# Performance work log

Measured on AMD Instinct MI355X. Metric: run time of the kernel, lower is better.

Reference implementation:

```python
import jax, jax.numpy as jnp
import numpy as np

N_HEAD = 16
ROPE_BASE = 10000.0


def _rotate_half(x):
    # interleaved rotate: (-x2, x1) pairs, matching torch stack+flatten
    x1 = x[..., ::2]
    x2 = x[..., 1::2]
    return jnp.stack((-x2, x1), axis=-1).reshape(x.shape)


def setup_inputs() -> dict:
    key = jax.random.key(0)
    ks = jax.random.split(key, 5)
    B, S, C = 4, 2048, 1024
    sc = 1.0 / np.sqrt(C)
    return {
        "x": jax.random.normal(ks[0], (B, S, C), jnp.float32),
        "W_qkv": jax.random.normal(ks[1], (C, 3 * C), jnp.float32) * sc,
        "b_qkv": jax.random.normal(ks[2], (3 * C,), jnp.float32) * 0.02,
        "W_proj": jax.random.normal(ks[3], (C, C), jnp.float32) * sc,
        "b_proj": jax.random.normal(ks[4], (C,), jnp.float32) * 0.02,
    }


def reference(x, W_qkv, b_qkv, W_proj, b_proj):
    B, S, C = x.shape
    H = N_HEAD
    D = C // H

    qkv = x @ W_qkv + b_qkv                       # [B,S,3C]
    q, k, v = jnp.split(qkv, 3, axis=-1)
    q = q.reshape(B, S, H, D).transpose(0, 2, 1, 3)  # [B,H,S,D]
    k = k.reshape(B, S, H, D).transpose(0, 2, 1, 3)
    v = v.reshape(B, S, H, D).transpose(0, 2, 1, 3)

    # RoPE cache (offset=0), faithful to source: emb = cat(freqs, freqs)
    inv_freq = 1.0 / (ROPE_BASE ** (jnp.arange(0, D, 2, dtype=jnp.float32) / D))
    pos = jnp.arange(S, dtype=jnp.float32)
    freqs = jnp.outer(pos, inv_freq)              # [S, D/2]
    emb = jnp.concatenate((freqs, freqs), axis=-1)  # [S, D]
    cos = jnp.cos(emb)[None, None, :, :]
    sin = jnp.sin(emb)[None, None, :, :]

    q = q * cos + _rotate_half(q) * sin
    k = k * cos + _rotate_half(k) * sin

    scale = 1.0 / jnp.sqrt(jnp.asarray(D, x.dtype))
    scores = jnp.einsum("bhqd,bhkd->bhqk", q, k) * scale  # [B,H,S,S]
    causal = jnp.tril(jnp.ones((S, S), dtype=bool))
    scores = jnp.where(causal[None, None], scores, jnp.asarray(-jnp.inf, x.dtype))
    att = jax.nn.softmax(scores, axis=-1)
    out = jnp.einsum("bhqk,bhkd->bhqd", att, v)    # [B,H,S,D]

    out = out.transpose(0, 2, 1, 3).reshape(B, S, C)
    out = out @ W_proj + b_proj                    # dropout=0 (eval)
    return out
```

## Files before the change

kernel.cpp:

```cpp
#include <hip/hip_runtime.h>
#include <hip/hip_bf16.h>
#include <math.h>

#define B_ 4
#define S_ 2048
#define C_ 1024
#define H_ 16
#define D_ 64
#define M_ (B_*S_)
#define NQKV (3*C_)
#define KDIM C_

typedef float f32x4 __attribute__((ext_vector_type(4)));
typedef float f32x16 __attribute__((ext_vector_type(16)));
typedef short bf16x8 __attribute__((ext_vector_type(8)));

static __device__ __forceinline__ ushort f2bf(float f){
    __hip_bfloat16 h = __float2bfloat16(f);
    union { __hip_bfloat16 b; ushort u; } v; v.b = h;
    return v.u;
}

static __device__ __forceinline__ void gload16(const ushort* g, ushort* l){
    __builtin_amdgcn_global_load_lds((__attribute__((address_space(1))) void*)g,
                                     (__attribute__((address_space(3))) void*)l,
                                     16, 0, 0);
}

__global__ void k_prep(const float* __restrict__ x, const float* __restrict__ Wqkv,
                       const float* __restrict__ Wproj,
                       ushort* __restrict__ xb, ushort* __restrict__ wqt,
                       ushort* __restrict__ wpt, unsigned* __restrict__ csT){
    __shared__ float tile[32][33];
    int blk = blockIdx.x, tid = threadIdx.x;
    if (blk < 2048){
        const int n4 = M_*KDIM/4;
        for (int i = blk*256 + tid; i < n4; i += 2048*256){
            float4 v = *(const float4*)(x + (size_t)i*4);
            ushort4 o = { f2bf(v.x), f2bf(v.y), f2bf(v.z), f2bf(v.w) };
            *(ushort4*)(xb + (size_t)i*4) = o;
        }
    } else if (blk < 5120){
        int t = blk - 2048;
        int c0 = (t % 96)*32, r0 = (t / 96)*32;
        int tx = tid & 31, ty = tid >> 5;
        for (int j = ty; j < 32; j += 8)
            tile[j][tx] = Wqkv[(size_t)(r0 + j)*NQKV + c0 + tx];
        __syncthreads();
        for (int j = ty; j < 32; j += 8)
            wqt[(size_t)(c0 + tx)*KDIM + r0 + j] = f2bf(tile[j][tx]);
    } else if (blk < 6144){
        int t = blk - 5120;
        int c0 = (t & 31)*32, r0 = (t >> 5)*32;
        int tx = tid & 31, ty = tid >> 5;
        for (int j = ty; j < 32; j += 8)
            tile[j][tx] = Wproj[(size_t)(r0 + j)*C_ + c0 + tx];
        __syncthreads();
        for (int j = ty; j < 32; j += 8)
            wpt[(size_t)(c0 + tx)*KDIM + r0 + j] = f2bf(tile[j][tx]);
    } else {
        int t = (blk - 6144)*256 + tid;
        int pos = t >> 6, d = t & 63;
        float invf = powf(10000.0f, -(float)(d & 31) / 32.0f);
        float ang = (float)pos * invf;
        csT[t] = (unsigned)f2bf(cosf(ang)) | ((unsigned)f2bf(sinf(ang)) << 16);
    }
}

__launch_bounds__(512, 4)
__global__ void k_qkv(const ushort* __restrict__ xb, const ushort* __restrict__ wt,
                      const float* __restrict__ bqkv, const unsigned* __restrict__ csT,
                      ushort* __restrict__ qb, ushort* __restrict__ kb, ushort* __restrict__ vT){
    __shared__ __align__(16) ushort As[2][256][32];
    __shared__ __align__(16) ushort Bs[2][128][32];
    int bid = blockIdx.x;
    int lin = (bid & 7)*96 + (bid >> 3);
    int bx = lin % 24, by = lin / 24;
    int M0 = by*256, N0 = bx*128;
    int tid = threadIdx.x;
    int wid = tid >> 6, lane = tid & 63;
    int wm = wid >> 1, wn = wid & 1;
    int lrow = lane & 15, lk = lane >> 4;
    int swu = (lrow >> 1) & 3;

    int scol = (((lane & 3) ^ ((lane >> 3) & 3))) * 8;
    const ushort* gA0 = &xb[(size_t)(M0 + wid*16 + (lane >> 2))*KDIM + scol];
    const ushort* gA1 = gA0 + (size_t)128*KDIM;
    const ushort* gB0 = &wt[(size_t)(N0 + wid*16 + (lane >> 2))*KDIM + scol];

    f32x4 acc[4][4] = {};
    int cur = 0;
    gload16(gA0, &As[0][wid*16][0]);
    gload16(gA1, &As[0][128 + wid*16][0]);
    gload16(gB0, &Bs[0][wid*16][0]);
    __syncthreads();

    for (int k0 = 0; k0 < KDIM; k0 += 32){
        int nk = k0 + 32;
        if (nk < KDIM){
            gload16(gA0 + nk, &As[cur^1][wid*16][0]);
            gload16(gA1 + nk, &As[cur^1][128 + wid*16][0]);
            gload16(gB0 + nk, &Bs[cur^1][wid*16][0]);
        }
        bf16x8 a[4], b[4];
#pragma unroll
        for (int mi = 0; mi < 4; mi++)
            a[mi] = *(const bf16x8*)(&As[cur][wm*64 + mi*16 + lrow][(lk ^ swu)*8]);
#pragma unroll
        for (int ni = 0; ni < 4; ni++)
            b[ni] = *(const bf16x8*)(&Bs[cur][wn*64 + ni*16 + lrow][(lk ^ swu)*8]);
#pragma unroll
        for (int mi = 0; mi < 4; mi++)
#pragma unroll
            for (int ni = 0; ni < 4; ni++)
                acc[mi][ni] = __builtin_amdgcn_mfma_f32_16x16x32_bf16(a[mi], b[ni], acc[mi][ni], 0, 0, 0);
        __syncthreads();
        cur ^= 1;
    }
#pragma unroll
    for (int mi = 0; mi < 4; mi++)
#pragma unroll
    for (int ni = 0; ni < 4; ni++){
        int gn = N0 + wn*64 + ni*16 + lrow;
        float bias = bqkv[gn];
        int which = gn >> 10;
        int cn = gn & 1023;
        int h = cn >> 6, d = cn & 63;
        int gm0 = M0 + wm*64 + mi*16 + lk*4;
        int bb = gm0 >> 11, pos0 = gm0 & 2047;
        if (which == 2){
            ushort4 o = { f2bf(acc[mi][ni][0] + bias), f2bf(acc[mi][ni][1] + bias),
                          f2bf(acc[mi][ni][2] + bias), f2bf(acc[mi][ni][3] + bias) };
            *(ushort4*)(&vT[(((size_t)(bb*H_ + h))*D_ + d)*S_ + pos0]) = o;
        } else {
#pragma unroll
            for (int rr = 0; rr < 4; rr++){
                float val = acc[mi][ni][rr] + bias;
                float rot = __shfl_xor(val, 1);
                unsigned cs = csT[(pos0 + rr)*64 + d];
                float c = __uint_as_float(cs << 16);
                float s = __uint_as_float(cs & 0xffff0000u);
                float o = val*c + ((d & 1) ? rot : -rot)*s;
                if (which == 0) o *= 0.18033688f;
                int out_idx = (((bb*H_ + h)*S_) + pos0 + rr)*D_ + d;
                ((which == 0) ? qb : kb)[out_idx] = f2bf(o);
            }
        }
    }
}

__launch_bounds__(512, 4)
__global__ void k_proj(const ushort* __restrict__ ab, const ushort* __restrict__ wt,
                       const float* __restrict__ bias, float* __restrict__ out){
    __shared__ __align__(16) ushort As[2][256][32];
    __shared__ __align__(16) ushort Bs[2][128][32];
    int bid = blockIdx.x;
    int lin = (bid & 7)*32 + (bid >> 3);
    int bx = lin & 7, by = lin >> 3;
    int M0 = by*256, N0 = bx*128;
    int tid = threadIdx.x;
    int wid = tid >> 6, lane = tid & 63;
    int wm = wid >> 1, wn = wid & 1;
    int lrow = lane & 15, lk = lane >> 4;
    int swu = (lrow >> 1) & 3;

    int scol = (((lane & 3) ^ ((lane >> 3) & 3))) * 8;
    const ushort* gA0 = &ab[(size_t)(M0 + wid*16 + (lane >> 2))*KDIM + scol];
    const ushort* gA1 = gA0 + (size_t)128*KDIM;
    const ushort* gB0 = &wt[(size_t)(N0 + wid*16 + (lane >> 2))*KDIM + scol];

    f32x4 acc[4][4] = {};
    int cur = 0;
    gload16(gA0, &As[0][wid*16][0]);
    gload16(gA1, &As[0][128 + wid*16][0]);
    gload16(gB0, &Bs[0][wid*16][0]);
    __syncthreads();

    for (int k0 = 0; k0 < KDIM; k0 += 32){
        int nk = k0 + 32;
        if (nk < KDIM){
            gload16(gA0 + nk, &As[cur^1][wid*16][0]);
            gload16(gA1 + nk, &As[cur^1][128 + wid*16][0]);
            gload16(gB0 + nk, &Bs[cur^1][wid*16][0]);
        }
        bf16x8 a[4], b[4];
#pragma unroll
        for (int mi = 0; mi < 4; mi++)
            a[mi] = *(const bf16x8*)(&As[cur][wm*64 + mi*16 + lrow][(lk ^ swu)*8]);
#pragma unroll
        for (int ni = 0; ni < 4; ni++)
            b[ni] = *(const bf16x8*)(&Bs[cur][wn*64 + ni*16 + lrow][(lk ^ swu)*8]);
#pragma unroll
        for (int mi = 0; mi < 4; mi++)
#pragma unroll
            for (int ni = 0; ni < 4; ni++)
                acc[mi][ni] = __builtin_amdgcn_mfma_f32_16x16x32_bf16(a[mi], b[ni], acc[mi][ni], 0, 0, 0);
        __syncthreads();
        cur ^= 1;
    }
#pragma unroll
    for (int mi = 0; mi < 4; mi++)
#pragma unroll
    for (int ni = 0; ni < 4; ni++){
        int gn = N0 + wn*64 + ni*16 + lrow;
        float bv = bias[gn];
#pragma unroll
        for (int rr = 0; rr < 4; rr++){
            int gm = M0 + wm*64 + mi*16 + lk*4 + rr;
            out[(size_t)gm*C_ + gn] = acc[mi][ni][rr] + bv;
        }
    }
}

__launch_bounds__(512, 2)
__global__ void k_attn(const ushort* __restrict__ qb, const ushort* __restrict__ kb,
                       const ushort* __restrict__ vT, ushort* __restrict__ ob){
    __shared__ __align__(16) ushort Ks[64][64];
    __shared__ __align__(16) ushort Vs[64][64];
    int bh = blockIdx.x;
    int qt = (gridDim.y - 1) - blockIdx.y;
    int bb = bh >> 4, h = bh & 15;
    int tid = threadIdx.x, wid = tid >> 6, lane = tid & 63;
    int lq = lane & 31, hi = lane >> 5;
    const ushort* qp = qb + (size_t)bh*S_*D_;
    const ushort* kp = kb + (size_t)bh*S_*D_;
    const ushort* vp = vT + (size_t)bh*D_*S_;
    int qw = qt*256 + wid*32;
    int qrow = qw + lq;
    int swz = lq & 7;

    bf16x8 fq[4];
#pragma unroll
    for (int c = 0; c < 4; c++)
        fq[c] = *(const bf16x8*)(&qp[qrow*D_ + c*16 + hi*8]);

    f32x16 acc0 = {}, acc1 = {};
    float l = 0.0f;

    int sr = tid >> 3, su = tid & 7;
    int swr = (su ^ (sr & 7)) * 8;
    int sc = su * 8;

    int4 ra = *(const int4*)(&kp[sr*D_ + sc]);
    int4 rc = *(const int4*)(&vp[(size_t)sr*S_ + sc]);

    int nit = 4*qt + 4;
    for (int it = 0; it < nit; ++it){
        int j0 = it*64;
        *(int4*)(&Ks[sr][swr]) = ra;
        *(int4*)(&Vs[sr][swr]) = rc;
        __syncthreads();
        if (it + 1 < nit){
            int j1 = j0 + 64;
            ra = *(const int4*)(&kp[(j1+sr)*D_ + sc]);
            rc = *(const int4*)(&vp[(size_t)sr*S_ + j1 + sc]);
        }
        int rel = qw - j0;
        if (rel >= 0){
            bool diag0 = (rel == 0);
            bool have1 = (rel >= 32);
            bool diag1 = (rel == 32);
            f32x16 z0 = {}, z1 = {};
            __builtin_amdgcn_s_setprio(1);
#pragma unroll
            for (int c = 0; c < 4; c++){
                bf16x8 kf = *(const bf16x8*)(&Ks[lq][((2*c + hi) ^ swz)*8]);
                z0 = __builtin_amdgcn_mfma_f32_32x32x16_bf16(kf, fq[c], z0, 0, 0, 0);
            }
            if (have1){
#pragma unroll
                for (int c = 0; c < 4; c++){
                    bf16x8 kf = *(const bf16x8*)(&Ks[32 + lq][((2*c + hi) ^ swz)*8]);
                    z1 = __builtin_amdgcn_mfma_f32_32x32x16_bf16(kf, fq[c], z1, 0, 0, 0);
                }
            }
            __builtin_amdgcn_s_setprio(0);
            if (diag0){
#pragma unroll
                for (int r = 0; r < 16; r++)
                    if (((r & 3) + 8*(r >> 2) + 4*hi) > lq) z0[r] = -1e30f;
            }
            if (diag1){
#pragma unroll
                for (int r = 0; r < 16; r++)
                    if (((r & 3) + 8*(r >> 2) + 4*hi) > lq) z1[r] = -1e30f;
            }
#pragma unroll
            for (int r = 0; r < 16; r++){ z0[r] = exp2f(z0[r]); l += z0[r]; }
            if (have1){
#pragma unroll
                for (int r = 0; r < 16; r++){ z1[r] = exp2f(z1[r]); l += z1[r]; }
            }

#define PV_SUB(zz, r0_, su_, t_) do {                                             \
    unsigned w0, w1, w2, w3;                                                      \
    asm("v_cvt_pk_bf16_f32 %0, %1, %2" : "=v"(w0) : "v"(zz[r0_+0]), "v"(zz[r0_+1])); \
    asm("v_cvt_pk_bf16_f32 %0, %1, %2" : "=v"(w1) : "v"(zz[r0_+2]), "v"(zz[r0_+3])); \
    asm("v_cvt_pk_bf16_f32 %0, %1, %2" : "=v"(w2) : "v"(zz[r0_+4]), "v"(zz[r0_+5])); \
    asm("v_cvt_pk_bf16_f32 %0, %1, %2" : "=v"(w3) : "v"(zz[r0_+6]), "v"(zz[r0_+7])); \
    auto s02 = __builtin_amdgcn_permlane32_swap(w0, w2, false, false);             \
    auto s13 = __builtin_amdgcn_permlane32_swap(w1, w3, false, false);             \
    union { unsigned u[4]; bf16x8 v; } pf;                                        \
    pf.u[0] = s02[0]; pf.u[1] = s13[0]; pf.u[2] = s02[1]; pf.u[3] = s13[1];       \
    bf16x8 vf0 = *(const bf16x8*)(&Vs[lq][(((su_)*4 + (t_)*2 + hi) ^ swz)*8]);    \
    acc0 = __builtin_amdgcn_mfma_f32_32x32x16_bf16(vf0, pf.v, acc0, 0, 0, 0);     \
    bf16x8 vf1 = *(const bf16x8*)(&Vs[32 + lq][(((su_)*4 + (t_)*2 + hi) ^ swz)*8]);\
    acc1 = __builtin_amdgcn_mfma_f32_32x32x16_bf16(vf1, pf.v, acc1, 0, 0, 0);     \
} while(0)

            __builtin_amdgcn_s_setprio(1);
            PV_SUB(z0, 0, 0, 0);
            PV_SUB(z0, 8, 0, 1);
            if (have1){
                PV_SUB(z1, 0, 1, 0);
                PV_SUB(z1, 8, 1, 1);
            }
            __builtin_amdgcn_s_setprio(0);
#undef PV_SUB
        }
        __syncthreads();
    }
    float lt = l + __shfl_xor(l, 32);
    float rl = 1.0f / lt;
#pragma unroll
    for (int rg = 0; rg < 4; rg++){
        ushort4 o0 = { f2bf(acc0[rg*4+0]*rl), f2bf(acc0[rg*4+1]*rl),
                       f2bf(acc0[rg*4+2]*rl), f2bf(acc0[rg*4+3]*rl) };
        *(ushort4*)(&ob[((size_t)(bb*S_ + qrow))*C_ + h*D_ + rg*8 + hi*4]) = o0;
        ushort4 o1 = { f2bf(acc1[rg*4+0]*rl), f2bf(acc1[rg*4+1]*rl),
                       f2bf(acc1[rg*4+2]*rl), f2bf(acc1[rg*4+3]*rl) };
        *(ushort4*)(&ob[((size_t)(bb*S_ + qrow))*C_ + h*D_ + 32 + rg*8 + hi*4]) = o1;
    }
}

extern "C" void kernel_launch(void* const* d_in, const int* in_sizes, int n_in,
                              void* d_out, int out_size, void* d_ws, size_t ws_size,
                              hipStream_t stream) {
    const float* x     = (const float*)d_in[0];
    const float* Wqkv  = (const float*)d_in[1];
    const float* bqkv  = (const float*)d_in[2];
    const float* Wproj = (const float*)d_in[3];
    const float* bproj = (const float*)d_in[4];
    float* out = (float*)d_out;

    char* ws = (char*)d_ws;
    ushort*   xb   = (ushort*)(ws);
    ushort*   wqt  = (ushort*)(ws + (16u<<20));
    ushort*   wpt  = (ushort*)(ws + (22u<<20));
    unsigned* csT  = (unsigned*)(ws + (24u<<20));
    ushort*   qbuf = (ushort*)(ws + (25u<<20));
    ushort*   kbuf = (ushort*)(ws + (41u<<20));
    ushort*   vbuf = (ushort*)(ws + (57u<<20));
    ushort*   obuf = (ushort*)(ws + (73u<<20));

    k_prep<<<6656, 256, 0, stream>>>(x, Wqkv, Wproj, xb, wqt, wpt, csT);
    k_qkv<<<768, 512, 0, stream>>>(xb, wqt, bqkv, csT, qbuf, kbuf, vbuf);
    k_attn<<<dim3(B_*H_, S_/256), 512, 0, stream>>>(qbuf, kbuf, vbuf, obuf);
    k_proj<<<256, 512, 0, stream>>>(obuf, wpt, bproj, out);
}
```

Measured before the change: 181.5 us.

## Double-buffer attention K/V tiles in LDS with direct global-to-LDS loads

The attention kernel previously prefetched the next K/V tile into registers, stored it to a single LDS buffer, and used two barriers per iteration. It now uses two LDS buffers, fills them with global_load_lds async copies (swizzle applied on the global address side), and keeps only one barrier per iteration. The aim is to overlap tile loading with the MFMA work, cut register pressure and the LDS store instructions, and halve the barrier count. The cost is doubled LDS use, which may limit occupancy. Correctness also depends on the barrier waiting for the outstanding async loads.

```diff
diff --git a/kernel.cpp b/kernel.cpp
--- a/kernel.cpp
+++ b/kernel.cpp
@@ -215,8 +215,8 @@
 __launch_bounds__(512, 2)
 __global__ void k_attn(const ushort* __restrict__ qb, const ushort* __restrict__ kb,
                        const ushort* __restrict__ vT, ushort* __restrict__ ob){
-    __shared__ __align__(16) ushort Ks[64][64];
-    __shared__ __align__(16) ushort Vs[64][64];
+    __shared__ __align__(16) ushort Ks[2][64][64];
+    __shared__ __align__(16) ushort Vs[2][64][64];
     int bh = blockIdx.x;
     int qt = (gridDim.y - 1) - blockIdx.y;
     int bb = bh >> 4, h = bh & 15;
@@ -237,25 +237,27 @@
     f32x16 acc0 = {}, acc1 = {};
     float l = 0.0f;
 
-    int sr = tid >> 3, su = tid & 7;
-    int swr = (su ^ (sr & 7)) * 8;
-    int sc = su * 8;
-
-    int4 ra = *(const int4*)(&kp[sr*D_ + sc]);
-    int4 rc = *(const int4*)(&vp[(size_t)sr*S_ + sc]);
+    int sr8 = lane >> 3, su = lane & 7;
+    int sscol = (su ^ (sr8 & 7)) * 8;
+    const ushort* gK = kp + (size_t)(wid*8 + sr8)*D_ + sscol;
+    const ushort* gV = vp + (size_t)(wid*8 + sr8)*S_ + sscol;
+    ushort* lK = &Ks[0][wid*8][0];
+    ushort* lV = &Vs[0][wid*8][0];
+    const int BUFS = 64*64;
 
     int nit = 4*qt + 4;
+    gload16(gK, lK);
+    gload16(gV, lV);
+
     for (int it = 0; it < nit; ++it){
-        int j0 = it*64;
-        *(int4*)(&Ks[sr][swr]) = ra;
-        *(int4*)(&Vs[sr][swr]) = rc;
+        int b = it & 1;
         __syncthreads();
         if (it + 1 < nit){
-            int j1 = j0 + 64;
-            ra = *(const int4*)(&kp[(j1+sr)*D_ + sc]);
-            rc = *(const int4*)(&vp[(size_t)sr*S_ + j1 + sc]);
-        }
-        int rel = qw - j0;
+            int j1 = (it + 1)*64;
+            gload16(gK + (size_t)j1*D_, lK + (b^1)*BUFS);
+            gload16(gV + j1,            lV + (b^1)*BUFS);
+        }
+        int rel = qw - it*64;
         if (rel >= 0){
             bool diag0 = (rel == 0);
             bool have1 = (rel >= 32);
@@ -264,13 +266,13 @@
             __builtin_amdgcn_s_setprio(1);
 #pragma unroll
             for (int c = 0; c < 4; c++){
-                bf16x8 kf = *(const bf16x8*)(&Ks[lq][((2*c + hi) ^ swz)*8]);
+                bf16x8 kf = *(const bf16x8*)(&Ks[b][lq][((2*c + hi) ^ swz)*8]);
                 z0 = __builtin_amdgcn_mfma_f32_32x32x16_bf16(kf, fq[c], z0, 0, 0, 0);
             }
             if (have1){
 #pragma unroll
                 for (int c = 0; c < 4; c++){
-                    bf16x8 kf = *(const bf16x8*)(&Ks[32 + lq][((2*c + hi) ^ swz)*8]);
+                    bf16x8 kf = *(const bf16x8*)(&Ks[b][32 + lq][((2*c + hi) ^ swz)*8]);
                     z1 = __builtin_amdgcn_mfma_f32_32x32x16_bf16(kf, fq[c], z1, 0, 0, 0);
                 }
             }
@@ -302,9 +304,9 @@
     auto s13 = __builtin_amdgcn_permlane32_swap(w1, w3, false, false);             \
     union { unsigned u[4]; bf16x8 v; } pf;                                        \
     pf.u[0] = s02[0]; pf.u[1] = s13[0]; pf.u[2] = s02[1]; pf.u[3] = s13[1];       \
-    bf16x8 vf0 = *(const bf16x8*)(&Vs[lq][(((su_)*4 + (t_)*2 + hi) ^ swz)*8]);    \
+    bf16x8 vf0 = *(const bf16x8*)(&Vs[b][lq][(((su_)*4 + (t_)*2 + hi) ^ swz)*8]);  \
     acc0 = __builtin_amdgcn_mfma_f32_32x32x16_bf16(vf0, pf.v, acc0, 0, 0, 0);     \
-    bf16x8 vf1 = *(const bf16x8*)(&Vs[32 + lq][(((su_)*4 + (t_)*2 + hi) ^ swz)*8]);\
+    bf16x8 vf1 = *(const bf16x8*)(&Vs[b][32 + lq][(((su_)*4 + (t_)*2 + hi) ^ swz)*8]);\
     acc1 = __builtin_amdgcn_mfma_f32_32x32x16_bf16(vf1, pf.v, acc1, 0, 0, 0);     \
 } while(0)
 
@@ -318,7 +320,6 @@
             __builtin_amdgcn_s_setprio(0);
 #undef PV_SUB
         }
-        __syncthreads();
     }
     float lt = l + __shfl_xor(l, 32);
     float rl = 1.0f / lt;
```

After: 184.6 us. No clear change (+1.7%).
